# Optimization experiments

Measured on AMD Instinct MI355X. Metric: run time of the kernel, lower is better.

## Reference

```python
import jax, jax.numpy as jnp
import numpy as np

GROUPS = 8
EPS = 1e-5


def setup_inputs() -> dict:
    key = jax.random.key(0)
    k1, k2, k3 = jax.random.split(key, 3)
    B, C, H, W = 4, 256, 64, 64
    x = jax.random.normal(k1, (B, C, H, W), dtype=jnp.float32)
    gamma = jnp.ones((C,), dtype=jnp.float32)
    beta = jnp.zeros((C,), dtype=jnp.float32)
    # conv1x1 weights flattened to [out, in]
    w_qkv = jax.random.normal(k2, (3 * C, C), dtype=jnp.float32) * (C ** -0.5)
    w_proj = jax.random.normal(k3, (C, C), dtype=jnp.float32) * (C ** -0.5)
    b_proj = jnp.zeros((C,), dtype=jnp.float32)
    return {"x": x, "gamma": gamma, "beta": beta, "w_qkv": w_qkv,
            "w_proj": w_proj, "b_proj": b_proj}


def group_norm(x, gamma, beta):
    B, C, H, W = x.shape
    xr = x.reshape(B, GROUPS, C // GROUPS, H * W)
    mu = xr.mean(axis=(2, 3), keepdims=True)
    var = xr.var(axis=(2, 3), keepdims=True)
    xn = (xr - mu) * jax.lax.rsqrt(var + EPS)
    xn = xn.reshape(B, C, H * W)
    return xn * gamma[None, :, None] + beta[None, :, None]


def reference(x, gamma, beta, w_qkv, w_proj, b_proj):
    B, C, H, W = x.shape
    N = H * W
    xn = group_norm(x, gamma, beta)               # [B, C, N]
    qkv = jnp.einsum('oc,bcn->bon', w_qkv, xn)    # [B, 3C, N]
    q, k, v = jnp.split(qkv, 3, axis=1)           # each [B, C, N]
    # attn[b, n, m] = sum_c q[b,c,n] * k[b,c,m] * C^-0.5
    scores = jnp.einsum('bcn,bcm->bnm', q, k) * (C ** -0.5)  # [B, N, N]
    attn = jax.nn.softmax(scores, axis=-1)
    # out = v @ attn^T  -> out[b,c,n] = sum_m v[b,c,m] * attn[b,n,m]
    out = jnp.einsum('bcm,bnm->bcn', v, attn)     # [B, C, N]
    y = jnp.einsum('oc,bcn->bon', w_proj, out) + b_proj[None, :, None]
    return x + y.reshape(B, C, H, W)
```

## Files before the change

### kernel.cpp

```cpp
#include <hip/hip_runtime.h>
#include <hip/hip_bf16.h>

#define BB 4
#define CC 256
#define NN 4096
#define GG 8
#define SPLITS 4
#define MBLK 64
#define TKV 32
#define ITERS (NN / SPLITS / TKV)

typedef unsigned char u8;
typedef unsigned short u16;
typedef unsigned int u32;
typedef __bf16 b16x8 __attribute__((ext_vector_type(8)));
typedef float f32x4 __attribute__((ext_vector_type(4)));
typedef u32 u32x4 __attribute__((ext_vector_type(4)));
typedef u32 u32x2 __attribute__((ext_vector_type(2)));
typedef u16 u16x4 __attribute__((ext_vector_type(4)));

#define QS 0.09016844005556021f
#define FMAX 8.0f


__device__ __forceinline__ u16 f2bf(float f) {
    u32 u = __builtin_bit_cast(u32, f);
    u = (u + 0x7FFFu + ((u >> 16) & 1u)) >> 16;
    return (u16)u;
}

__device__ __forceinline__ float bf2f(u16 h) {
    return __builtin_bit_cast(float, (u32)h << 16);
}

__device__ __forceinline__ u32 pack_bf2(float a, float b) {
    float2 f; f.x = a; f.y = b;
    __hip_bfloat162 h = __float22bfloat162_rn(f);
    u32 r;
    __builtin_memcpy(&r, &h, 4);
    return r;
}

__device__ __forceinline__ float exp2_raw(float x) {
#if __has_builtin(__builtin_amdgcn_exp2f)
    return __builtin_amdgcn_exp2f(x);
#else
    float r;
    asm("v_exp_f32 %0, %1" : "=v"(r) : "v"(x));
    return r;
#endif
}

__device__ __forceinline__ b16x8 ldfrag(const u16* p) {
    u32x4 v = *reinterpret_cast<const u32x4*>(p);
    return __builtin_bit_cast(b16x8, v);
}

__device__ __forceinline__ int pk_fp8x4(float a, float b, float c, float d) {
    int r = __builtin_amdgcn_cvt_pk_fp8_f32(a, b, 0, false);
    r = __builtin_amdgcn_cvt_pk_fp8_f32(c, d, r, true);
    return r;
}

__device__ __forceinline__ long as_long(u32x2 v) { return __builtin_bit_cast(long, v); }

typedef __attribute__((address_space(1))) const unsigned int* gas_p;
typedef __attribute__((address_space(3))) unsigned int* las_p;

__device__ __forceinline__ void g2l(const u8* g, u8* l) {
    __builtin_amdgcn_global_load_lds((gas_p)g, (las_p)l, 16, 0, 0);
}

__global__ void fold_w(const float* __restrict__ w_qkv, const float* __restrict__ w_proj,
                       const float* __restrict__ gamma, const float* __restrict__ beta,
                       const float* __restrict__ stats,
                       u16* __restrict__ wqf, float* __restrict__ biasq,
                       u16* __restrict__ wpf) {
    int o = blockIdx.x;
    int b = blockIdx.y;
    int c = threadIdx.x;
    int g = c >> 5;
    float mu   = stats[(b * GG + g) * 2];
    float rstd = stats[(b * GG + g) * 2 + 1];
    float a  = gamma[c] * rstd;
    float bb = beta[c] - mu * a;
    float w = w_qkv[o * CC + c];
    size_t fe = ((size_t)((o >> 4) * 8 + (c >> 5)) * 64 + ((c & 31) >> 3) * 16 + (o & 15)) * 8 + (c & 7);
    wqf[(size_t)b * 768 * CC + fe] = f2bf(w * a);
    float part = w * bb;
    #pragma unroll
    for (int off = 32; off; off >>= 1) part += __shfl_down(part, off, 64);
    __shared__ float red[4];
    if ((threadIdx.x & 63) == 0) red[threadIdx.x >> 6] = part;
    __syncthreads();
    if (threadIdx.x == 0) biasq[b * 768 + o] = red[0] + red[1] + red[2] + red[3];
    if (b == 0 && o < CC) {
        float wp = w_proj[o * CC + c];
        wpf[fe] = f2bf(wp);
    }
}

__global__ void transpose_x(const float* __restrict__ x, u16* __restrict__ xtf,
                            float* __restrict__ gsum) {
    __shared__ float tile[64][65];
    __shared__ float red[4][4];
    int n0 = blockIdx.x * 64, c0 = blockIdx.y * 64, b = blockIdx.z;
    int t = threadIdx.x;
    int col = t & 63, r0 = t >> 6;
    const float* xp = x + (size_t)b * CC * NN;
    float s0 = 0.f, ss0 = 0.f, s1 = 0.f, ss1 = 0.f;
    #pragma unroll
    for (int i = 0; i < 16; ++i) {
        int row = i * 4 + r0;
        float v = xp[(size_t)(c0 + row) * NN + n0 + col];
        tile[row][col] = v;
        if (i < 8) { s0 += v; ss0 += v * v; } else { s1 += v; ss1 += v * v; }
    }
    #pragma unroll
    for (int off = 32; off; off >>= 1) {
        s0 += __shfl_down(s0, off, 64); ss0 += __shfl_down(ss0, off, 64);
        s1 += __shfl_down(s1, off, 64); ss1 += __shfl_down(ss1, off, 64);
    }
    int wid = t >> 6;
    if ((t & 63) == 0) { red[wid][0] = s0; red[wid][1] = ss0; red[wid][2] = s1; red[wid][3] = ss1; }
    __syncthreads();
    if (t < 2) {
        float s  = red[0][t * 2] + red[1][t * 2] + red[2][t * 2] + red[3][t * 2];
        float ss = red[0][t * 2 + 1] + red[1][t * 2 + 1] + red[2][t * 2 + 1] + red[3][t * 2 + 1];
        int g = (c0 >> 5) + t;
        atomicAdd(&gsum[(b * GG + g) * 2], s);
        atomicAdd(&gsum[(b * GG + g) * 2 + 1], ss);
    }
    int nl = t >> 2;
    int cbq = t & 3;
    int l15 = nl & 15;
    int ntile = (n0 >> 4) + (nl >> 4);
    int kk = (c0 >> 5) + (cbq >> 1);
    u16* ob = xtf + (size_t)b * NN * CC;
    #pragma unroll
    for (int g = 0; g < 4; ++g) {
        int quad = (cbq & 1) * 2 + (g >> 1);
        int j0 = (g & 1) * 4;
        u16x4 v;
        v.x = f2bf(tile[cbq * 16 + g * 4 + 0][nl]);
        v.y = f2bf(tile[cbq * 16 + g * 4 + 1][nl]);
        v.z = f2bf(tile[cbq * 16 + g * 4 + 2][nl]);
        v.w = f2bf(tile[cbq * 16 + g * 4 + 3][nl]);
        *reinterpret_cast<u16x4*>(ob + ((size_t)(ntile * 8 + kk) * 64 + quad * 16 + l15) * 8 + j0) = v;
    }
}

__global__ void gn_finalize(const float* __restrict__ gsum, float* __restrict__ stats) {
    int i = threadIdx.x;
    if (i < BB * GG) {
        float s = gsum[i * 2], ss = gsum[i * 2 + 1];
        const float inv = 1.f / ((CC / GG) * NN);
        float mu = s * inv;
        float var = ss * inv - mu * mu;
        stats[i * 2] = mu;
        stats[i * 2 + 1] = rsqrtf(var + 1e-5f);
    }
}

__global__ void __launch_bounds__(256) qkv_gemm(const u16* __restrict__ wqf,
                                                const float* __restrict__ biasq,
                                                const u16* __restrict__ xtf,
                                                u8* __restrict__ qtf, u8* __restrict__ ktf,
                                                u8* __restrict__ vvf) {
    int b = blockIdx.z;
    int o0 = blockIdx.y * 64;
    int n0 = blockIdx.x * 64;
    int lane = threadIdx.x & 63, w = threadIdx.x >> 6;
    int l15 = lane & 15, quad = lane >> 4;
    const u16* A  = wqf + (size_t)b * 768 * CC;
    const u16* Bp = xtf + (size_t)b * NN * CC;
    int otile = (o0 >> 4) + w;
    f32x4 acc[4] = {};
    #pragma unroll
    for (int kk = 0; kk < 8; ++kk) {
        b16x8 af = ldfrag(A + (size_t)(otile * 8 + kk) * 512 + lane * 8);
        #pragma unroll
        for (int nt = 0; nt < 4; ++nt) {
            b16x8 bf = ldfrag(Bp + (size_t)(((n0 >> 4) + nt) * 8 + kk) * 512 + lane * 8);
            acc[nt] = __builtin_amdgcn_mfma_f32_16x16x32_bf16(af, bf, acc[nt], 0, 0, 0);
        }
    }
    int o_base = o0 + w * 16 + quad * 4;
    float bias[4];
    #pragma unroll
    for (int r = 0; r < 4; ++r) bias[r] = biasq[b * 768 + o_base + r];

    if (o0 < 512) {
        int oloc = (o0 < 256) ? o_base : (o_base - 256);
        u8* dst = ((o0 < 256) ? qtf : ktf) + (size_t)b * NN * CC;
        #pragma unroll
        for (int nt = 0; nt < 4; ++nt) {
            int n = n0 + nt * 16 + l15;
            int pk = pk_fp8x4(acc[nt][0] + bias[0], acc[nt][1] + bias[1],
                              acc[nt][2] + bias[2], acc[nt][3] + bias[3]);
            size_t addr = (size_t)((n >> 4) * 4 + (oloc >> 6)) * 1024
                        + ((oloc & 31) >> 3) * 256 + (n & 15) * 16
                        + ((oloc >> 5) & 1) * 8 + (oloc & 7);
            *reinterpret_cast<u32*>(dst + addr) = (u32)pk;
        }
    } else {
        int cb = o_base - 512;
        u8* dst = vvf + (size_t)b * NN * CC;
        #pragma unroll
        for (int nt = 0; nt < 4; ++nt) {
            int kv = n0 + nt * 16 + l15;
            int pk = pk_fp8x4(acc[nt][0] + bias[0], acc[nt][1] + bias[1],
                              acc[nt][2] + bias[2], acc[nt][3] + bias[3]);
            size_t base = (size_t)((kv >> 5) * 8 + (cb >> 5)) * 1024
                        + ((kv & 31) >> 3) * 256 + ((cb >> 4) & 1) * 8 + (kv & 7);
            #pragma unroll
            for (int r = 0; r < 4; ++r)
                dst[base + ((cb & 15) + r) * 16] = (u8)(pk >> (r * 8));
        }
    }
}

__global__ void __launch_bounds__(256, 4) flash(const u8* __restrict__ qtf,
                                                const u8* __restrict__ ktf,
                                                const u8* __restrict__ vvf,
                                                u16* __restrict__ po,
                                                float* __restrict__ lp) {
    __shared__ u8 kbuf[2][8192];
    __shared__ u8 vbuf[2][8192];
    __shared__ u8 pbuf[4][16 * 40];
    int lin = blockIdx.x;
    int chunk = lin & 15;
    int nblk = lin >> 4;
    int b = chunk >> 2, sp = chunk & 3;
    int lane = threadIdx.x & 63, w = threadIdx.x >> 6;
    int l15 = lane & 15, quad = lane >> 4;
    int ntile = nblk * 4 + w;
    const u8* kb8 = ktf + (size_t)b * NN * CC;
    const u8* vb8 = vvf + (size_t)b * NN * CC;
    u8* pw = &pbuf[w][0];

    const u32x2 ones2 = {0x38383838u, 0x38383838u};
    const long ones8 = as_long(ones2);

    u32x4 aq[4];
    const u8* qb = qtf + (size_t)b * NN * CC + (size_t)ntile * 4096;
    #pragma unroll
    for (int s = 0; s < 4; ++s)
        aq[s] = *reinterpret_cast<const u32x4*>(qb + s * 1024 + lane * 16);

    f32x4 acco[16] = {};
    f32x4 acco_l = {};

    const int m_beg = sp * (NN / SPLITS);

    auto stage = [&](int buf, int m0) {
        const u8* ks = kb8 + ((size_t)m0 << 8);
        const u8* vs = vb8 + ((size_t)m0 << 8);
        #pragma unroll
        for (int j = 0; j < 4; ++j) {
            int idx = w * 4 + j;
            if (idx < 8) g2l(ks + idx * 1024 + lane * 16, &kbuf[buf][idx * 1024]);
            else         g2l(vs + (idx - 8) * 1024 + lane * 16, &vbuf[buf][(idx - 8) * 1024]);
        }
    };

    stage(0, m_beg);
    __syncthreads();
    for (int it = 0; it < ITERS; ++it) {
        int cur = it & 1;
        if (it + 1 < ITERS) stage(cur ^ 1, m_beg + (it + 1) * TKV);
        const u8* kc = &kbuf[cur][0];
        const u8* vc = &vbuf[cur][0];
        f32x4 accs[2] = {};
        #pragma unroll
        for (int s = 0; s < 4; ++s) {
            long alo = as_long(u32x2{aq[s].x, aq[s].y});
            long ahi = as_long(u32x2{aq[s].z, aq[s].w});
            #pragma unroll
            for (int m = 0; m < 2; ++m) {
                u32x4 kf = *reinterpret_cast<const u32x4*>(kc + (size_t)(m * 4 + s) * 1024 + lane * 16);
                accs[m] = __builtin_amdgcn_mfma_f32_16x16x32_fp8_fp8(
                    alo, as_long(u32x2{kf.x, kf.y}), accs[m], 0, 0, 0);
                accs[m] = __builtin_amdgcn_mfma_f32_16x16x32_fp8_fp8(
                    ahi, as_long(u32x2{kf.z, kf.w}), accs[m], 0, 0, 0);
            }
        }
        #pragma unroll
        for (int m = 0; m < 2; ++m) {
            float e0 = exp2_raw(fmaf(accs[m][0], QS, -FMAX));
            float e1 = exp2_raw(fmaf(accs[m][1], QS, -FMAX));
            float e2 = exp2_raw(fmaf(accs[m][2], QS, -FMAX));
            float e3 = exp2_raw(fmaf(accs[m][3], QS, -FMAX));
            int p01 = __builtin_amdgcn_cvt_pk_fp8_f32(e0, e1, 0, false);
            int p23 = __builtin_amdgcn_cvt_pk_fp8_f32(e2, e3, 0, false);
            u8* pr = pw + m * 16 + l15;
            pr[(quad * 4 + 0) * 40] = (u8)p01;
            pr[(quad * 4 + 1) * 40] = (u8)(p01 >> 8);
            pr[(quad * 4 + 2) * 40] = (u8)p23;
            pr[(quad * 4 + 3) * 40] = (u8)(p23 >> 8);
        }
        asm volatile("s_waitcnt lgkmcnt(0)" ::: "memory");
        u32x2 apv = *reinterpret_cast<const u32x2*>(pw + l15 * 40 + quad * 8);
        long ap = as_long(apv);
        acco_l = __builtin_amdgcn_mfma_f32_16x16x32_fp8_fp8(ap, ones8, acco_l, 0, 0, 0);
        #pragma unroll
        for (int c2 = 0; c2 < 8; ++c2) {
            u32x4 vf = *reinterpret_cast<const u32x4*>(vc + (size_t)c2 * 1024 + lane * 16);
            acco[c2 * 2]     = __builtin_amdgcn_mfma_f32_16x16x32_fp8_fp8(
                ap, as_long(u32x2{vf.x, vf.y}), acco[c2 * 2], 0, 0, 0);
            acco[c2 * 2 + 1] = __builtin_amdgcn_mfma_f32_16x16x32_fp8_fp8(
                ap, as_long(u32x2{vf.z, vf.w}), acco[c2 * 2 + 1], 0, 0, 0);
        }
        __syncthreads();
    }
    u16* pochunk = po + ((size_t)(sp * BB + b) * 256 + ntile) * 4096;
    #pragma unroll
    for (int ct = 0; ct < 16; ++ct) {
        u32x2 st;
        st.x = pack_bf2(acco[ct][0], acco[ct][1]);
        st.y = pack_bf2(acco[ct][2], acco[ct][3]);
        *reinterpret_cast<u32x2*>(pochunk + (size_t)(ct * 64 + quad * 16 + l15) * 4) = st;
    }
    if (l15 == 0) {
        size_t lbase = (size_t)(sp * BB + b) * NN + ntile * 16;
        #pragma unroll
        for (int r = 0; r < 4; ++r) lp[lbase + quad * 4 + r] = acco_l[r];
    }
}

__global__ void __launch_bounds__(256) combine(const u16* __restrict__ po,
                                               const float* __restrict__ lp,
                                               u16* __restrict__ otf) {
    int idx = blockIdx.x * 256 + threadIdx.x;
    int cg   = idx & 31;
    int quad = (idx >> 5) & 3;
    int nb   = (idx >> 7) & 255;
    int b    = idx >> 15;
    float acc[4][8] = {};
    float lsum[4] = {};
    #pragma unroll
    for (int s = 0; s < SPLITS; ++s) {
        const u16* src = po + (((size_t)(s * BB + b) * 256 + nb) * 4096)
                       + ((cg >> 1) * 256 + quad * 64 + (cg & 1) * 32);
        u16 s16[32];
        #pragma unroll
        for (int q = 0; q < 4; ++q)
            *reinterpret_cast<u32x4*>(&s16[q * 8]) = *reinterpret_cast<const u32x4*>(src + q * 8);
        #pragma unroll
        for (int r = 0; r < 4; ++r)
            #pragma unroll
            for (int j = 0; j < 8; ++j)
                acc[r][j] += bf2f(s16[j * 4 + r]);
        #pragma unroll
        for (int r = 0; r < 4; ++r)
            lsum[r] += lp[(size_t)(s * BB + b) * NN + nb * 16 + quad * 4 + r];
    }
    u16* dstb = otf + (size_t)b * NN * CC;
    #pragma unroll
    for (int r = 0; r < 4; ++r) {
        float inv = 1.f / lsum[r];
        u16 outv[8];
        #pragma unroll
        for (int j = 0; j < 8; ++j) outv[j] = f2bf(acc[r][j] * inv);
        size_t off = ((size_t)(nb * 8 + (cg >> 2)) * 64 + (cg & 3) * 16 + quad * 4 + r) * 8;
        *reinterpret_cast<u32x4*>(dstb + off) = *reinterpret_cast<const u32x4*>(outv);
    }
}

__global__ void __launch_bounds__(256) proj(const u16* __restrict__ wpf,
                                            const float* __restrict__ b_proj,
                                            const u16* __restrict__ otf,
                                            const float* __restrict__ x,
                                            float* __restrict__ out) {
    int b = blockIdx.z, o0 = blockIdx.y * 64, n0 = blockIdx.x * 64;
    int lane = threadIdx.x & 63, w = threadIdx.x >> 6;
    int l15 = lane & 15, quad = lane >> 4;
    const u16* Bp = otf + (size_t)b * NN * CC;
    int otile = (o0 >> 4) + w;
    f32x4 acc[4] = {};
    #pragma unroll
    for (int kk = 0; kk < 8; ++kk) {
        b16x8 af = ldfrag(wpf + (size_t)(otile * 8 + kk) * 512 + lane * 8);
        #pragma unroll
        for (int nt = 0; nt < 4; ++nt) {
            b16x8 bf = ldfrag(Bp + (size_t)(((n0 >> 4) + nt) * 8 + kk) * 512 + lane * 8);
            acc[nt] = __builtin_amdgcn_mfma_f32_16x16x32_bf16(af, bf, acc[nt], 0, 0, 0);
        }
    }
    int o_base = o0 + w * 16 + quad * 4;
    #pragma unroll
    for (int nt = 0; nt < 4; ++nt) {
        int n = n0 + nt * 16 + l15;
        #pragma unroll
        for (int r = 0; r < 4; ++r) {
            int o = o_base + r;
            size_t idx = ((size_t)(b * CC + o)) * NN + n;
            out[idx] = acc[nt][r] + b_proj[o] + x[idx];
        }
    }
}

extern "C" void kernel_launch(void* const* d_in, const int* in_sizes, int n_in,
                              void* d_out, int out_size, void* d_ws, size_t ws_size,
                              hipStream_t stream) {
    const float* x      = (const float*)d_in[0];
    const float* gamma  = (const float*)d_in[1];
    const float* beta   = (const float*)d_in[2];
    const float* w_qkv  = (const float*)d_in[3];
    const float* w_proj = (const float*)d_in[4];
    const float* b_proj = (const float*)d_in[5];
    float* out = (float*)d_out;

    char* p = (char*)d_ws;
    float* stats = (float*)p; p += 256;
    float* gsum  = (float*)p; p += 256;
    float* biasq = (float*)p; p += (size_t)BB * 768 * sizeof(float);
    u16* wqf = (u16*)p; p += (size_t)BB * 768 * CC * 2;
    u16* wpf = (u16*)p; p += (size_t)CC * CC * 2;
    u16* xtf = (u16*)p; p += (size_t)BB * NN * CC * 2;
    u8* qtf8 = (u8*)p; p += (size_t)BB * NN * CC;
    u8* ktf8 = (u8*)p; p += (size_t)BB * NN * CC;
    u8* vvf8 = (u8*)p; p += (size_t)BB * NN * CC;
    u16* otf = (u16*)p; p += (size_t)BB * NN * CC * 2;
    u16* po = (u16*)p; p += (size_t)SPLITS * BB * NN * CC * 2;
    float* lp = (float*)p; p += (size_t)SPLITS * BB * NN * sizeof(float);
    (void)ws_size; (void)in_sizes; (void)n_in; (void)out_size;

    (void)hipMemsetAsync(gsum, 0, BB * GG * 2 * sizeof(float), stream);
    transpose_x<<<dim3(NN / 64, CC / 64, BB), 256, 0, stream>>>(x, xtf, gsum);
    gn_finalize<<<1, 64, 0, stream>>>(gsum, stats);
    fold_w<<<dim3(768, BB), 256, 0, stream>>>(w_qkv, w_proj, gamma, beta, stats, wqf, biasq, wpf);
    qkv_gemm<<<dim3(NN / 64, 12, BB), 256, 0, stream>>>(wqf, biasq, xtf, qtf8, ktf8, vvf8);
    flash<<<(NN / MBLK) * SPLITS * BB, 256, 0, stream>>>(qtf8, ktf8, vvf8, po, lp);
    combine<<<(BB * NN * CC / 32) / 256, 256, 0, stream>>>(po, lp, otf);
    proj<<<dim3(NN / 64, CC / 64, BB), 256, 0, stream>>>(wpf, b_proj, otf, x, out);
}
```

Before: 195.1 us.

## Enlarge flash tiles to 128 queries and 64 keys, stage X in LDS for QKV GEMM

The flash kernel now runs 512 threads (8 waves) per block covering 128 query rows and steps through 64 keys per iteration. This doubles reuse of each staged K/V tile and halves the number of barriers per key range. The QKV GEMM now stages the X tile in LDS once and computes 128 output channels per block, so X reuse doubles and global loads drop. The cost is larger LDS use (64KB for flash), higher register pressure from the extra accumulators, and half as many blocks in both kernels, which reduces occupancy and parallelism.

```diff
diff --git a/kernel.cpp b/kernel.cpp
--- a/kernel.cpp
+++ b/kernel.cpp
@@ -6,8 +6,7 @@
 #define NN 4096
 #define GG 8
 #define SPLITS 4
-#define MBLK 64
-#define TKV 32
+#define TKV 64
 #define ITERS (NN / SPLITS / TKV)
 
 typedef unsigned char u8;
@@ -68,6 +67,10 @@
 typedef __attribute__((address_space(3))) unsigned int* las_p;
 
 __device__ __forceinline__ void g2l(const u8* g, u8* l) {
+    __builtin_amdgcn_global_load_lds((gas_p)g, (las_p)l, 16, 0, 0);
+}
+
+__device__ __forceinline__ void g2l16(const u16* g, u16* l) {
     __builtin_amdgcn_global_load_lds((gas_p)g, (las_p)l, 16, 0, 0);
 }
 
@@ -167,74 +170,89 @@
                                                 const u16* __restrict__ xtf,
                                                 u8* __restrict__ qtf, u8* __restrict__ ktf,
                                                 u8* __restrict__ vvf) {
+    __shared__ u16 bx[16384];
     int b = blockIdx.z;
-    int o0 = blockIdx.y * 64;
+    int o0 = blockIdx.y * 128;
     int n0 = blockIdx.x * 64;
     int lane = threadIdx.x & 63, w = threadIdx.x >> 6;
     int l15 = lane & 15, quad = lane >> 4;
-    const u16* A  = wqf + (size_t)b * 768 * CC;
-    const u16* Bp = xtf + (size_t)b * NN * CC;
-    int otile = (o0 >> 4) + w;
-    f32x4 acc[4] = {};
+    const u16* Bg = xtf + (size_t)b * NN * CC + (size_t)n0 * 256;
+    #pragma unroll
+    for (int j = 0; j < 8; ++j) {
+        int c = w * 8 + j;
+        g2l16(Bg + (size_t)c * 512 + lane * 8, bx + (size_t)c * 512 + lane * 8);
+    }
+    __syncthreads();
+
+    const u16* A = wqf + (size_t)b * 768 * CC;
+    f32x4 acc[2][4] = {};
     #pragma unroll
     for (int kk = 0; kk < 8; ++kk) {
-        b16x8 af = ldfrag(A + (size_t)(otile * 8 + kk) * 512 + lane * 8);
+        b16x8 af[2];
+        #pragma unroll
+        for (int t = 0; t < 2; ++t) {
+            int otile = (o0 >> 4) + w * 2 + t;
+            af[t] = ldfrag(A + (size_t)(otile * 8 + kk) * 512 + lane * 8);
+        }
         #pragma unroll
         for (int nt = 0; nt < 4; ++nt) {
-            b16x8 bf = ldfrag(Bp + (size_t)(((n0 >> 4) + nt) * 8 + kk) * 512 + lane * 8);
-            acc[nt] = __builtin_amdgcn_mfma_f32_16x16x32_bf16(af, bf, acc[nt], 0, 0, 0);
-        }
-    }
-    int o_base = o0 + w * 16 + quad * 4;
-    float bias[4];
-    #pragma unroll
-    for (int r = 0; r < 4; ++r) bias[r] = biasq[b * 768 + o_base + r];
-
-    if (o0 < 512) {
-        int oloc = (o0 < 256) ? o_base : (o_base - 256);
-        u8* dst = ((o0 < 256) ? qtf : ktf) + (size_t)b * NN * CC;
-        #pragma unroll
-        for (int nt = 0; nt < 4; ++nt) {
-            int n = n0 + nt * 16 + l15;
-            int pk = pk_fp8x4(acc[nt][0] + bias[0], acc[nt][1] + bias[1],
-                              acc[nt][2] + bias[2], acc[nt][3] + bias[3]);
-            size_t addr = (size_t)((n >> 4) * 4 + (oloc >> 6)) * 1024
-                        + ((oloc & 31) >> 3) * 256 + (n & 15) * 16
-                        + ((oloc >> 5) & 1) * 8 + (oloc & 7);
-            *reinterpret_cast<u32*>(dst + addr) = (u32)pk;
-        }
-    } else {
-        int cb = o_base - 512;
-        u8* dst = vvf + (size_t)b * NN * CC;
-        #pragma unroll
-        for (int nt = 0; nt < 4; ++nt) {
-            int kv = n0 + nt * 16 + l15;
-            int pk = pk_fp8x4(acc[nt][0] + bias[0], acc[nt][1] + bias[1],
-                              acc[nt][2] + bias[2], acc[nt][3] + bias[3]);
-            size_t base = (size_t)((kv >> 5) * 8 + (cb >> 5)) * 1024
-                        + ((kv & 31) >> 3) * 256 + ((cb >> 4) & 1) * 8 + (kv & 7);
+            b16x8 bf = ldfrag(bx + (size_t)(nt * 8 + kk) * 512 + lane * 8);
+            acc[0][nt] = __builtin_amdgcn_mfma_f32_16x16x32_bf16(af[0], bf, acc[0][nt], 0, 0, 0);
+            acc[1][nt] = __builtin_amdgcn_mfma_f32_16x16x32_bf16(af[1], bf, acc[1][nt], 0, 0, 0);
+        }
+    }
+    #pragma unroll
+    for (int t = 0; t < 2; ++t) {
+        int o_base = o0 + (w * 2 + t) * 16 + quad * 4;
+        float bias[4];
+        #pragma unroll
+        for (int r = 0; r < 4; ++r) bias[r] = biasq[b * 768 + o_base + r];
+        if (o0 < 512) {
+            int oloc = (o0 < 256) ? o_base : (o_base - 256);
+            u8* dst = ((o0 < 256) ? qtf : ktf) + (size_t)b * NN * CC;
             #pragma unroll
-            for (int r = 0; r < 4; ++r)
-                dst[base + ((cb & 15) + r) * 16] = (u8)(pk >> (r * 8));
-        }
-    }
-}
-
-__global__ void __launch_bounds__(256, 4) flash(const u8* __restrict__ qtf,
+            for (int nt = 0; nt < 4; ++nt) {
+                int n = n0 + nt * 16 + l15;
+                int pk = pk_fp8x4(acc[t][nt][0] + bias[0], acc[t][nt][1] + bias[1],
+                                  acc[t][nt][2] + bias[2], acc[t][nt][3] + bias[3]);
+                size_t addr = (size_t)((n >> 4) * 4 + (oloc >> 6)) * 1024
+                            + ((oloc & 31) >> 3) * 256 + (n & 15) * 16
+                            + ((oloc >> 5) & 1) * 8 + (oloc & 7);
+                *reinterpret_cast<u32*>(dst + addr) = (u32)pk;
+            }
+        } else {
+            int cb = o_base - 512;
+            u8* dst = vvf + (size_t)b * NN * CC;
+            #pragma unroll
+            for (int nt = 0; nt < 4; ++nt) {
+                int kv = n0 + nt * 16 + l15;
+                int pk = pk_fp8x4(acc[t][nt][0] + bias[0], acc[t][nt][1] + bias[1],
+                                  acc[t][nt][2] + bias[2], acc[t][nt][3] + bias[3]);
+                size_t base = (size_t)((kv >> 5) * 8 + (cb >> 5)) * 1024
+                            + ((kv & 31) >> 3) * 256 + ((cb >> 4) & 1) * 8 + (kv & 7);
+                #pragma unroll
+                for (int r = 0; r < 4; ++r)
+                    dst[base + ((cb & 15) + r) * 16] = (u8)(pk >> (r * 8));
+            }
+        }
+    }
+}
+
+__global__ void __launch_bounds__(512, 4) flash(const u8* __restrict__ qtf,
                                                 const u8* __restrict__ ktf,
                                                 const u8* __restrict__ vvf,
                                                 u16* __restrict__ po,
                                                 float* __restrict__ lp) {
-    __shared__ u8 kbuf[2][8192];
-    __shared__ u8 vbuf[2][8192];
-    __shared__ u8 pbuf[4][16 * 40];
+    __shared__ u8 kbuf[2][16384];
+    __shared__ u8 vbuf[2][16384];
+    __shared__ u8 pbuf[8][16 * 72];
     int lin = blockIdx.x;
     int chunk = lin & 15;
     int nblk = lin >> 4;
     int b = chunk >> 2, sp = chunk & 3;
     int lane = threadIdx.x & 63, w = threadIdx.x >> 6;
     int l15 = lane & 15, quad = lane >> 4;
-    int ntile = nblk * 4 + w;
+    int ntile = nblk * 8 + w;
     const u8* kb8 = ktf + (size_t)b * NN * CC;
     const u8* vb8 = vvf + (size_t)b * NN * CC;
     u8* pw = &pbuf[w][0];
@@ -259,8 +277,8 @@
         #pragma unroll
         for (int j = 0; j < 4; ++j) {
             int idx = w * 4 + j;
-            if (idx < 8) g2l(ks + idx * 1024 + lane * 16, &kbuf[buf][idx * 1024]);
-            else         g2l(vs + (idx - 8) * 1024 + lane * 16, &vbuf[buf][(idx - 8) * 1024]);
+            if (idx < 16) g2l(ks + idx * 1024 + lane * 16, &kbuf[buf][idx * 1024]);
+            else          g2l(vs + (idx - 16) * 1024 + lane * 16, &vbuf[buf][(idx - 16) * 1024]);
         }
     };
 
@@ -271,13 +289,13 @@
         if (it + 1 < ITERS) stage(cur ^ 1, m_beg + (it + 1) * TKV);
         const u8* kc = &kbuf[cur][0];
         const u8* vc = &vbuf[cur][0];
-        f32x4 accs[2] = {};
+        f32x4 accs[4] = {};
         #pragma unroll
         for (int s = 0; s < 4; ++s) {
             long alo = as_long(u32x2{aq[s].x, aq[s].y});
             long ahi = as_long(u32x2{aq[s].z, aq[s].w});
             #pragma unroll
-            for (int m = 0; m < 2; ++m) {
+            for (int m = 0; m < 4; ++m) {
                 u32x4 kf = *reinterpret_cast<const u32x4*>(kc + (size_t)(m * 4 + s) * 1024 + lane * 16);
                 accs[m] = __builtin_amdgcn_mfma_f32_16x16x32_fp8_fp8(
                     alo, as_long(u32x2{kf.x, kf.y}), accs[m], 0, 0, 0);
@@ -286,7 +304,7 @@
             }
         }
         #pragma unroll
-        for (int m = 0; m < 2; ++m) {
+        for (int m = 0; m < 4; ++m) {
             float e0 = exp2_raw(fmaf(accs[m][0], QS, -FMAX));
             float e1 = exp2_raw(fmaf(accs[m][1], QS, -FMAX));
             float e2 = exp2_raw(fmaf(accs[m][2], QS, -FMAX));
@@ -294,22 +312,28 @@
             int p01 = __builtin_amdgcn_cvt_pk_fp8_f32(e0, e1, 0, false);
             int p23 = __builtin_amdgcn_cvt_pk_fp8_f32(e2, e3, 0, false);
             u8* pr = pw + m * 16 + l15;
-            pr[(quad * 4 + 0) * 40] = (u8)p01;
-            pr[(quad * 4 + 1) * 40] = (u8)(p01 >> 8);
-            pr[(quad * 4 + 2) * 40] = (u8)p23;
-            pr[(quad * 4 + 3) * 40] = (u8)(p23 >> 8);
+            pr[(quad * 4 + 0) * 72] = (u8)p01;
+            pr[(quad * 4 + 1) * 72] = (u8)(p01 >> 8);
+            pr[(quad * 4 + 2) * 72] = (u8)p23;
+            pr[(quad * 4 + 3) * 72] = (u8)(p23 >> 8);
         }
         asm volatile("s_waitcnt lgkmcnt(0)" ::: "memory");
-        u32x2 apv = *reinterpret_cast<const u32x2*>(pw + l15 * 40 + quad * 8);
-        long ap = as_long(apv);
-        acco_l = __builtin_amdgcn_mfma_f32_16x16x32_fp8_fp8(ap, ones8, acco_l, 0, 0, 0);
+        long ap0 = as_long(*reinterpret_cast<const u32x2*>(pw + l15 * 72 + quad * 8));
+        long ap1 = as_long(*reinterpret_cast<const u32x2*>(pw + l15 * 72 + 32 + quad * 8));
+        acco_l = __builtin_amdgcn_mfma_f32_16x16x32_fp8_fp8(ap0, ones8, acco_l, 0, 0, 0);
+        acco_l = __builtin_amdgcn_mfma_f32_16x16x32_fp8_fp8(ap1, ones8, acco_l, 0, 0, 0);
         #pragma unroll
         for (int c2 = 0; c2 < 8; ++c2) {
-            u32x4 vf = *reinterpret_cast<const u32x4*>(vc + (size_t)c2 * 1024 + lane * 16);
+            u32x4 vf0 = *reinterpret_cast<const u32x4*>(vc + (size_t)c2 * 1024 + lane * 16);
+            u32x4 vf1 = *reinterpret_cast<const u32x4*>(vc + (size_t)(8 + c2) * 1024 + lane * 16);
             acco[c2 * 2]     = __builtin_amdgcn_mfma_f32_16x16x32_fp8_fp8(
-                ap, as_long(u32x2{vf.x, vf.y}), acco[c2 * 2], 0, 0, 0);
+                ap0, as_long(u32x2{vf0.x, vf0.y}), acco[c2 * 2], 0, 0, 0);
             acco[c2 * 2 + 1] = __builtin_amdgcn_mfma_f32_16x16x32_fp8_fp8(
-                ap, as_long(u32x2{vf.z, vf.w}), acco[c2 * 2 + 1], 0, 0, 0);
+                ap0, as_long(u32x2{vf0.z, vf0.w}), acco[c2 * 2 + 1], 0, 0, 0);
+            acco[c2 * 2]     = __builtin_amdgcn_mfma_f32_16x16x32_fp8_fp8(
+                ap1, as_long(u32x2{vf1.x, vf1.y}), acco[c2 * 2], 0, 0, 0);
+            acco[c2 * 2 + 1] = __builtin_amdgcn_mfma_f32_16x16x32_fp8_fp8(
+                ap1, as_long(u32x2{vf1.z, vf1.w}), acco[c2 * 2 + 1], 0, 0, 0);
         }
         __syncthreads();
     }
@@ -430,8 +454,8 @@
     transpose_x<<<dim3(NN / 64, CC / 64, BB), 256, 0, stream>>>(x, xtf, gsum);
     gn_finalize<<<1, 64, 0, stream>>>(gsum, stats);
     fold_w<<<dim3(768, BB), 256, 0, stream>>>(w_qkv, w_proj, gamma, beta, stats, wqf, biasq, wpf);
-    qkv_gemm<<<dim3(NN / 64, 12, BB), 256, 0, stream>>>(wqf, biasq, xtf, qtf8, ktf8, vvf8);
-    flash<<<(NN / MBLK) * SPLITS * BB, 256, 0, stream>>>(qtf8, ktf8, vvf8, po, lp);
+    qkv_gemm<<<dim3(NN / 64, 6, BB), 256, 0, stream>>>(wqf, biasq, xtf, qtf8, ktf8, vvf8);
+    flash<<<(NN / 128) * SPLITS * BB, 512, 0, stream>>>(qtf8, ktf8, vvf8, po, lp);
     combine<<<(BB * NN * CC / 32) / 256, 256, 0, stream>>>(po, lp, otf);
     proj<<<dim3(NN / 64, CC / 64, BB), 256, 0, stream>>>(wpf, b_proj, otf, x, out);
 }
```

Result: faster. 185.0 us (-5.2%).
